# Performance work log

Measured on AMD Instinct MI355X. Metric: run time of the kernel, lower is better.

## Reference

```python
import jax, jax.numpy as jnp
import numpy as np

B, S, D = 2, 2048, 768
H, STRIDE = 12, 8
HD = D // H  # 64


def setup_inputs() -> dict:
    key = jax.random.key(0)
    k0, k1, k2 = jax.random.split(key, 3)
    x = jax.random.normal(k0, (B, S, D), dtype=jnp.float32)
    qkv_w = jax.random.normal(k1, (3 * D, D), dtype=jnp.float32) * 0.02
    qkv_b = jnp.zeros((3 * D,), dtype=jnp.float32)
    out_w = jax.random.normal(k2, (D, D), dtype=jnp.float32) * 0.02
    out_b = jnp.zeros((D,), dtype=jnp.float32)
    return {"x": x, "qkv_w": qkv_w, "qkv_b": qkv_b, "out_w": out_w, "out_b": out_b}


def _stride_mask(S, stride, causal):
    i = jnp.arange(S)[:, None]
    j = jnp.arange(S)[None, :]
    strided = (j % stride == 0)
    if causal:
        strided = strided & (j <= i)
    # diagonal always attended; previous token attended for i > 0
    return strided | (j == i) | (j == i - 1)


def reference(x, qkv_w, qkv_b, out_w, out_b):
    Bx, Sx, Dx = x.shape
    qkv = x @ qkv_w.T + qkv_b                      # [B,S,3D]
    qkv = qkv.reshape(Bx, Sx, 3, H, HD)
    q, k, v = jnp.transpose(qkv, (2, 0, 3, 1, 4))  # each [B,H,S,HD]
    scale = HD ** -0.5
    attn = jnp.einsum('bhid,bhjd->bhij', q, k) * scale  # [B,H,S,S]
    mask = _stride_mask(Sx, STRIDE, True)          # [S,S] bool
    attn = jnp.where(mask[None, None], attn, -jnp.inf)
    a = jax.nn.softmax(attn, axis=-1)
    # every row has at least the diagonal unmasked, so no NaN rows;
    # nan_to_num kept for exact parity with the torch module
    a = jnp.nan_to_num(a, nan=0.0)
    out = jnp.einsum('bhij,bhjd->bhid', a, v)      # [B,H,S,HD]
    out = jnp.transpose(out, (0, 2, 1, 3)).reshape(Bx, Sx, Dx)
    return out @ out_w.T + out_b
```

## Files before the change

### kernel.cpp

```cpp
#include <hip/hip_runtime.h>
#include <hip/hip_bf16.h>
#include <stdint.h>

#define H_   12
#define S_   2048
#define D_   768
#define HD_  64
#define MS_  256

typedef __bf16 bf16_8 __attribute__((ext_vector_type(8)));
typedef float  f32_4  __attribute__((ext_vector_type(4)));

typedef __attribute__((address_space(1))) void* gas_ptr;
typedef __attribute__((address_space(3))) void* las_ptr;

__device__ __forceinline__ void g2l16(const void* g, void* l) {
  __builtin_amdgcn_global_load_lds((gas_ptr)g, (las_ptr)l, 16, 0, 0);
}

__device__ __forceinline__ f32_4 mfma16(bf16_8 a, bf16_8 b, f32_4 c) {
  return __builtin_amdgcn_mfma_f32_16x16x32_bf16(a, b, c, 0, 0, 0);
}

__device__ __forceinline__ bf16_8 ld8(const __hip_bfloat16* p) {
  return *reinterpret_cast<const bf16_8*>(p);
}

__global__ __launch_bounds__(256) void cvt3_f32_bf16(
    const float* __restrict__ a, const float* __restrict__ b,
    const float* __restrict__ c, __hip_bfloat16* __restrict__ out,
    int na4, int nb4) {
  const int t = blockIdx.x * 256 + threadIdx.x;
  float4 f;
  if (t < na4)            f = reinterpret_cast<const float4*>(a)[t];
  else if (t < na4 + nb4) f = reinterpret_cast<const float4*>(b)[t - na4];
  else                    f = reinterpret_cast<const float4*>(c)[t - na4 - nb4];
  union { __hip_bfloat16 h[4]; ushort4 u; } p;
  p.h[0] = __float2bfloat16(f.x);
  p.h[1] = __float2bfloat16(f.y);
  p.h[2] = __float2bfloat16(f.z);
  p.h[3] = __float2bfloat16(f.w);
  reinterpret_cast<ushort4*>(out)[t] = p.u;
}

template <int MODE, int BN>
__global__ __launch_bounds__(256, 2) void gemm_bt(
    const __hip_bfloat16* __restrict__ A, const __hip_bfloat16* __restrict__ B,
    const float* __restrict__ bias,
    __hip_bfloat16* __restrict__ O0, __hip_bfloat16* __restrict__ O1,
    __hip_bfloat16* __restrict__ O2, __hip_bfloat16* __restrict__ O3,
    __hip_bfloat16* __restrict__ O4, float* __restrict__ OF,
    int M, int N, int K) {
  constexpr int NTJ = BN / 32;
  __shared__ __bf16 sA[128 * 32];
  __shared__ __bf16 sB[BN * 32];
  const int tid  = threadIdx.x;
  const int lane = tid & 63;
  const int wv   = tid >> 6;
  const int m0 = blockIdx.y * 128;
  const int n0 = blockIdx.x * BN;
  const int wr = (wv >> 1) * 64;
  const int wc = (wv & 1) * (BN / 2);

  f32_4 acc[4][NTJ] = {};

  const __hip_bfloat16* aS = A + (size_t)(m0 + (tid >> 2)) * K + ((tid & 3) << 3);
  const __hip_bfloat16* bS = B + (size_t)(n0 + (tid >> 2)) * K + ((tid & 3) << 3);
  const size_t half = (size_t)64 * K;
  __bf16* dA  = &sA[tid * 8];
  __bf16* dA2 = &sA[tid * 8 + 2048];
  __bf16* dB  = &sB[tid * 8];
  __bf16* dB2 = &sB[tid * 8 + 2048];

  const int fr = lane & 15;
  const int kq = (lane >> 4) << 3;

  for (int k0 = 0; k0 < K; k0 += 32) {
    g2l16(aS, dA);
    g2l16(aS + half, dA2);
    g2l16(bS, dB);
    if constexpr (BN == 128) g2l16(bS + half, dB2);
    aS += 32;
    bS += 32;
    __syncthreads();
    bf16_8 af[4], bfm[NTJ];
#pragma unroll
    for (int t = 0; t < 4; ++t)
      af[t] = *reinterpret_cast<const bf16_8*>(&sA[(wr + t * 16 + fr) * 32 + kq]);
#pragma unroll
    for (int t = 0; t < NTJ; ++t)
      bfm[t] = *reinterpret_cast<const bf16_8*>(&sB[(wc + t * 16 + fr) * 32 + kq]);
#pragma unroll
    for (int ti = 0; ti < 4; ++ti)
#pragma unroll
      for (int tj = 0; tj < NTJ; ++tj)
        acc[ti][tj] = mfma16(af[ti], bfm[tj], acc[ti][tj]);
    __syncthreads();
  }

  const int crow = (lane >> 4) << 2;
  const int ccol = lane & 15;
#pragma unroll
  for (int ti = 0; ti < 4; ++ti) {
    const int gmb = m0 + wr + ti * 16 + crow;
#pragma unroll
    for (int tj = 0; tj < NTJ; ++tj) {
      const int gn = n0 + wc + tj * 16 + ccol;
      const float bv = bias[gn];
      if (MODE == 0) {
        const int t   = gn / D_;
        const int rem = gn - t * D_;
        const int hh = rem >> 6, dd = rem & 63;
        if (t < 2) {
          __hip_bfloat16* dst = (t == 0) ? O0 : O1;
#pragma unroll
          for (int r = 0; r < 4; ++r) {
            const int gm = gmb + r;
            const int bb = gm >> 11, ss = gm & (S_ - 1);
            const __hip_bfloat16 hv = __float2bfloat16(acc[ti][tj][r] + bv);
            dst[(((size_t)(bb * H_ + hh) << 11) + ss) * HD_ + dd] = hv;
            if (t == 1 && r == 0 && (gmb & 7) == 0)
              O4[(((size_t)(bb * H_ + hh)) * MS_ + (ss >> 3)) * HD_ + dd] = hv;
          }
        } else {
          const int bb = gmb >> 11, ss = gmb & (S_ - 1);
          union { ushort4 u; __hip_bfloat16 h[4]; } pk;
#pragma unroll
          for (int r = 0; r < 4; ++r) pk.h[r] = __float2bfloat16(acc[ti][tj][r] + bv);
          const size_t rowb = ((size_t)(bb * H_ + hh) * HD_ + dd);
          *reinterpret_cast<ushort4*>(O2 + rowb * S_ + ss) = pk.u;
          if ((ss & 7) == 0) O3[rowb * MS_ + (ss >> 3)] = pk.h[0];
        }
      } else {
#pragma unroll
        for (int r = 0; r < 4; ++r)
          OF[(size_t)(gmb + r) * D_ + gn] = acc[ti][tj][r] + bv;
      }
    }
  }
}

__global__ __launch_bounds__(256) void attn_mfma(
    const __hip_bfloat16* __restrict__ Q, const __hip_bfloat16* __restrict__ Kb,
    const __hip_bfloat16* __restrict__ Ks, const __hip_bfloat16* __restrict__ VT,
    const __hip_bfloat16* __restrict__ VsT, __hip_bfloat16* __restrict__ ctx) {
  __shared__ __bf16 pt[4][16 * 40];
  const int lane = threadIdx.x & 63;
  const int wv   = threadIdx.x >> 6;
  const int task = blockIdx.x * 4 + wv;
  const int bh   = task >> 7;
  const int i0   = (task & 127) << 4;
  const int lr   = lane & 15;
  const int quad = lane >> 4;
  const float SC = 0.125f * 1.44269504088896340736f;

  const __hip_bfloat16* Kh  = Kb  + ((size_t)bh << 11) * HD_;
  const __hip_bfloat16* Ksh = Ks  + (size_t)bh * MS_ * HD_;
  const __hip_bfloat16* VTh = VT  + (size_t)bh * HD_ * S_;
  const __hip_bfloat16* Vsh = VsT + (size_t)bh * HD_ * MS_;
  __bf16* ptw = pt[wv];

  const __hip_bfloat16* qp = Q + (((size_t)bh << 11) + i0 + lr) * HD_ + quad * 8;
  const bf16_8 qf0 = ld8(qp);
  const bf16_8 qf1 = ld8(qp + 32);

  const __bf16 one = (__bf16)1.0f;
  const bf16_8 onesf = {one, one, one, one, one, one, one, one};

  f32_4 Lacc = {}, oacc[4];
#pragma unroll
  for (int ct = 0; ct < 4; ++ct) oacc[ct] = f32_4{0.f, 0.f, 0.f, 0.f};

  const int mmax  = (i0 + 15) >> 3;
  const int nstr  = (mmax >> 5) + 1;
  const int jbase = (i0 >= 8) ? (i0 - 8) : 0;

  auto load_chunk = [&](int c, bf16_8 (&kf)[2][2], bf16_8 (&vf)[4]) {
    if (c < nstr) {
      const int mb = c << 5;
#pragma unroll
      for (int t = 0; t < 2; ++t) {
        const __hip_bfloat16* kp = Ksh + (size_t)(mb + t * 16 + lr) * HD_ + quad * 8;
        kf[t][0] = ld8(kp);
        kf[t][1] = ld8(kp + 32);
      }
#pragma unroll
      for (int ct = 0; ct < 4; ++ct)
        vf[ct] = ld8(Vsh + (size_t)(ct * 16 + lr) * MS_ + mb + quad * 8);
    } else {
#pragma unroll
      for (int t = 0; t < 2; ++t) {
        const int j  = jbase + t * 16 + lr;
        const int jr = (j < S_) ? j : (S_ - 1);
        const __hip_bfloat16* kp = Kh + (size_t)jr * HD_ + quad * 8;
        kf[t][0] = ld8(kp);
        kf[t][1] = ld8(kp + 32);
      }
      const int vs0 = jbase + quad * 8;
      const int vs  = (vs0 <= S_ - 8) ? vs0 : (S_ - 8);
#pragma unroll
      for (int ct = 0; ct < 4; ++ct)
        vf[ct] = ld8(VTh + (size_t)(ct * 16 + lr) * S_ + vs);
    }
  };

  bf16_8 kf[2][2], vf[4], kf2[2][2], vf2[4];
  load_chunk(0, kf, vf);

  for (int c = 0; c <= nstr; ++c) {
    if (c < nstr) load_chunk(c + 1, kf2, vf2);

    const bool strided = (c < nstr);
    const int  mb      = c << 5;

    f32_4 s0 = {}, s1 = {};
    s0 = mfma16(qf0, kf[0][0], s0);
    s0 = mfma16(qf1, kf[0][1], s0);
    s1 = mfma16(qf0, kf[1][0], s1);
    s1 = mfma16(qf1, kf[1][1], s1);

#pragma unroll
    for (int r = 0; r < 4; ++r) {
      const int i = i0 + quad * 4 + r;
      bool v0, v1;
      if (strided) {
        v0 = ((mb + lr) << 3) <= i;
        v1 = ((mb + 16 + lr) << 3) <= i;
      } else {
        const int j0 = jbase + lr, j1 = jbase + 16 + lr;
        v0 = (j0 == i || j0 == i - 1) && (j0 & 7);
        v1 = (j1 == i || j1 == i - 1) && (j1 & 7);
      }
      s0[r] = v0 ? exp2f(fminf(s0[r] * SC, 63.f)) : 0.f;
      s1[r] = v1 ? exp2f(fminf(s1[r] * SC, 63.f)) : 0.f;
    }

#pragma unroll
    for (int r = 0; r < 4; ++r) {
      const int row = quad * 4 + r;
      ptw[row * 40 + lr]      = (__bf16)__float2bfloat16(s0[r]);
      ptw[row * 40 + 16 + lr] = (__bf16)__float2bfloat16(s1[r]);
    }
    const bf16_8 pf = *reinterpret_cast<const bf16_8*>(&ptw[lr * 40 + quad * 8]);

#pragma unroll
    for (int ct = 0; ct < 4; ++ct) oacc[ct] = mfma16(pf, vf[ct], oacc[ct]);
    Lacc = mfma16(pf, onesf, Lacc);

    if (c < nstr) {
#pragma unroll
      for (int t = 0; t < 2; ++t) { kf[t][0] = kf2[t][0]; kf[t][1] = kf2[t][1]; }
#pragma unroll
      for (int ct = 0; ct < 4; ++ct) vf[ct] = vf2[ct];
    }
  }

  const int b = bh / H_;
  const int h = bh - b * H_;
  f32_4 inv;
#pragma unroll
  for (int r = 0; r < 4; ++r) inv[r] = 1.f / Lacc[r];
#pragma unroll
  for (int r = 0; r < 4; ++r) {
    const int i = i0 + quad * 4 + r;
    __hip_bfloat16* cp = ctx + ((size_t)(b * S_ + i)) * D_ + h * HD_ + lr;
#pragma unroll
    for (int ct = 0; ct < 4; ++ct)
      cp[ct * 16] = __float2bfloat16(oacc[ct][r] * inv[r]);
  }
}

extern "C" void kernel_launch(void* const* d_in, const int* in_sizes, int n_in,
                              void* d_out, int out_size, void* d_ws, size_t ws_size,
                              hipStream_t stream) {
  const float* x    = (const float*)d_in[0];
  const float* qkvw = (const float*)d_in[1];
  const float* qkvb = (const float*)d_in[2];
  const float* outw = (const float*)d_in[3];
  const float* outb = (const float*)d_in[4];
  float* out = (float*)d_out;

  const size_t NX  = (size_t)2 * S_ * D_;
  const size_t NW1 = (size_t)3 * D_ * D_;
  const size_t NW2 = (size_t)D_ * D_;
  const size_t NVS = (size_t)2 * H_ * HD_ * MS_;

  __hip_bfloat16* xb  = (__hip_bfloat16*)d_ws;
  __hip_bfloat16* w1b = xb + NX;
  __hip_bfloat16* w2b = w1b + NW1;
  __hip_bfloat16* q   = w2b + NW2;
  __hip_bfloat16* k   = q + NX;
  __hip_bfloat16* vt  = k + NX;
  __hip_bfloat16* vst = vt + NX;
  __hip_bfloat16* ks  = vst + NVS;
  __hip_bfloat16* ctx = ks + NVS;

  const int na4 = (int)(NX / 4), nb4 = (int)(NW1 / 4), nc4 = (int)(NW2 / 4);
  cvt3_f32_bf16<<<dim3((na4 + nb4 + nc4) / 256), 256, 0, stream>>>(
      x, qkvw, outw, xb, na4, nb4);

  gemm_bt<0, 128><<<dim3(2304 / 128, 4096 / 128), 256, 0, stream>>>(
      xb, w1b, qkvb, q, k, vt, vst, ks, nullptr, 4096, 2304, 768);

  attn_mfma<<<dim3(2 * H_ * S_ / 16 / 4), 256, 0, stream>>>(q, k, ks, vt, vst, ctx);

  gemm_bt<1, 64><<<dim3(768 / 64, 4096 / 128), 256, 0, stream>>>(
      ctx, w2b, outb, nullptr, nullptr, nullptr, nullptr, nullptr,
      out, 4096, 768, 768);
}
```

Before: 151.9 us.

## Store V row-major and transpose the local band through LDS in attention

The QKV GEMM epilogue now writes V in the same row-major [B,H,S,HD] layout as Q and K instead of a transposed [HD,S] layout with strided 4-element stores. The attention kernel stages the 32-row local V band into a per-wave LDS buffer and gathers the transposed MFMA fragments from there. The local-band chunk is also split out of the strided loop, removing the per-iteration branch on mask type. This trades scattered global stores in the GEMM for an extra 16 KB of LDS per block and element-wise LDS gathers in attention, which may reduce occupancy.

```diff
diff --git a/kernel.cpp b/kernel.cpp
--- a/kernel.cpp
+++ b/kernel.cpp
@@ -111,25 +111,19 @@
         const int t   = gn / D_;
         const int rem = gn - t * D_;
         const int hh = rem >> 6, dd = rem & 63;
-        if (t < 2) {
-          __hip_bfloat16* dst = (t == 0) ? O0 : O1;
-#pragma unroll
-          for (int r = 0; r < 4; ++r) {
-            const int gm = gmb + r;
-            const int bb = gm >> 11, ss = gm & (S_ - 1);
-            const __hip_bfloat16 hv = __float2bfloat16(acc[ti][tj][r] + bv);
-            dst[(((size_t)(bb * H_ + hh) << 11) + ss) * HD_ + dd] = hv;
-            if (t == 1 && r == 0 && (gmb & 7) == 0)
+        __hip_bfloat16* dst = (t == 0) ? O0 : (t == 1) ? O1 : O2;
+#pragma unroll
+        for (int r = 0; r < 4; ++r) {
+          const int gm = gmb + r;
+          const int bb = gm >> 11, ss = gm & (S_ - 1);
+          const __hip_bfloat16 hv = __float2bfloat16(acc[ti][tj][r] + bv);
+          dst[(((size_t)(bb * H_ + hh) << 11) + ss) * HD_ + dd] = hv;
+          if (r == 0 && (gmb & 7) == 0) {
+            if (t == 1)
               O4[(((size_t)(bb * H_ + hh)) * MS_ + (ss >> 3)) * HD_ + dd] = hv;
+            else if (t == 2)
+              O3[((size_t)(bb * H_ + hh) * HD_ + dd) * MS_ + (ss >> 3)] = hv;
           }
-        } else {
-          const int bb = gmb >> 11, ss = gmb & (S_ - 1);
-          union { ushort4 u; __hip_bfloat16 h[4]; } pk;
-#pragma unroll
-          for (int r = 0; r < 4; ++r) pk.h[r] = __float2bfloat16(acc[ti][tj][r] + bv);
-          const size_t rowb = ((size_t)(bb * H_ + hh) * HD_ + dd);
-          *reinterpret_cast<ushort4*>(O2 + rowb * S_ + ss) = pk.u;
-          if ((ss & 7) == 0) O3[rowb * MS_ + (ss >> 3)] = pk.h[0];
         }
       } else {
 #pragma unroll
@@ -142,9 +136,10 @@
 
 __global__ __launch_bounds__(256) void attn_mfma(
     const __hip_bfloat16* __restrict__ Q, const __hip_bfloat16* __restrict__ Kb,
-    const __hip_bfloat16* __restrict__ Ks, const __hip_bfloat16* __restrict__ VT,
+    const __hip_bfloat16* __restrict__ Ks, const __hip_bfloat16* __restrict__ Vr,
     const __hip_bfloat16* __restrict__ VsT, __hip_bfloat16* __restrict__ ctx) {
   __shared__ __bf16 pt[4][16 * 40];
+  __shared__ __bf16 vb[4][32 * 64];
   const int lane = threadIdx.x & 63;
   const int wv   = threadIdx.x >> 6;
   const int task = blockIdx.x * 4 + wv;
@@ -156,9 +151,31 @@
 
   const __hip_bfloat16* Kh  = Kb  + ((size_t)bh << 11) * HD_;
   const __hip_bfloat16* Ksh = Ks  + (size_t)bh * MS_ * HD_;
-  const __hip_bfloat16* VTh = VT  + (size_t)bh * HD_ * S_;
+  const __hip_bfloat16* Vrh = Vr  + ((size_t)bh << 11) * HD_;
   const __hip_bfloat16* Vsh = VsT + (size_t)bh * HD_ * MS_;
   __bf16* ptw = pt[wv];
+  __bf16* vbw = vb[wv];
+
+  const int jbase = (i0 >= 8) ? (i0 - 8) : 0;
+
+#pragma unroll
+  for (int it = 0; it < 4; ++it) {
+    const int cidx = it * 64 + lane;
+    const int row = cidx >> 3, seg = cidx & 7;
+    const int j  = jbase + row;
+    const int jr = (j < S_) ? j : (S_ - 1);
+    *reinterpret_cast<bf16_8*>(vbw + row * 64 + seg * 8) =
+        ld8(Vrh + (size_t)jr * HD_ + seg * 8);
+  }
+  bf16_8 kb_[2][2];
+#pragma unroll
+  for (int t = 0; t < 2; ++t) {
+    const int j  = jbase + t * 16 + lr;
+    const int jr = (j < S_) ? j : (S_ - 1);
+    const __hip_bfloat16* kp = Kh + (size_t)jr * HD_ + quad * 8;
+    kb_[t][0] = ld8(kp);
+    kb_[t][1] = ld8(kp + 32);
+  }
 
   const __hip_bfloat16* qp = Q + (((size_t)bh << 11) + i0 + lr) * HD_ + quad * 8;
   const bf16_8 qf0 = ld8(qp);
@@ -171,47 +188,41 @@
 #pragma unroll
   for (int ct = 0; ct < 4; ++ct) oacc[ct] = f32_4{0.f, 0.f, 0.f, 0.f};
 
-  const int mmax  = (i0 + 15) >> 3;
-  const int nstr  = (mmax >> 5) + 1;
-  const int jbase = (i0 >= 8) ? (i0 - 8) : 0;
-
-  auto load_chunk = [&](int c, bf16_8 (&kf)[2][2], bf16_8 (&vf)[4]) {
-    if (c < nstr) {
-      const int mb = c << 5;
-#pragma unroll
-      for (int t = 0; t < 2; ++t) {
-        const __hip_bfloat16* kp = Ksh + (size_t)(mb + t * 16 + lr) * HD_ + quad * 8;
-        kf[t][0] = ld8(kp);
-        kf[t][1] = ld8(kp + 32);
-      }
-#pragma unroll
-      for (int ct = 0; ct < 4; ++ct)
-        vf[ct] = ld8(Vsh + (size_t)(ct * 16 + lr) * MS_ + mb + quad * 8);
-    } else {
-#pragma unroll
-      for (int t = 0; t < 2; ++t) {
-        const int j  = jbase + t * 16 + lr;
-        const int jr = (j < S_) ? j : (S_ - 1);
-        const __hip_bfloat16* kp = Kh + (size_t)jr * HD_ + quad * 8;
-        kf[t][0] = ld8(kp);
-        kf[t][1] = ld8(kp + 32);
-      }
-      const int vs0 = jbase + quad * 8;
-      const int vs  = (vs0 <= S_ - 8) ? vs0 : (S_ - 8);
-#pragma unroll
-      for (int ct = 0; ct < 4; ++ct)
-        vf[ct] = ld8(VTh + (size_t)(ct * 16 + lr) * S_ + vs);
-    }
+  const int mmax = (i0 + 15) >> 3;
+  const int nstr = (mmax >> 5) + 1;
+
+  auto load_str = [&](int c, bf16_8 (&kf)[2][2], bf16_8 (&vf)[4]) {
+    const int mb = c << 5;
+#pragma unroll
+    for (int t = 0; t < 2; ++t) {
+      const __hip_bfloat16* kp = Ksh + (size_t)(mb + t * 16 + lr) * HD_ + quad * 8;
+      kf[t][0] = ld8(kp);
+      kf[t][1] = ld8(kp + 32);
+    }
+#pragma unroll
+    for (int ct = 0; ct < 4; ++ct)
+      vf[ct] = ld8(Vsh + (size_t)(ct * 16 + lr) * MS_ + mb + quad * 8);
   };
 
+  auto softmax_pv = [&](f32_4& s0, f32_4& s1, const bf16_8 (&vf)[4]) {
+#pragma unroll
+    for (int r = 0; r < 4; ++r) {
+      const int row = quad * 4 + r;
+      ptw[row * 40 + lr]      = (__bf16)__float2bfloat16(s0[r]);
+      ptw[row * 40 + 16 + lr] = (__bf16)__float2bfloat16(s1[r]);
+    }
+    const bf16_8 pf = *reinterpret_cast<const bf16_8*>(&ptw[lr * 40 + quad * 8]);
+#pragma unroll
+    for (int ct = 0; ct < 4; ++ct) oacc[ct] = mfma16(pf, vf[ct], oacc[ct]);
+    Lacc = mfma16(pf, onesf, Lacc);
+  };
+
   bf16_8 kf[2][2], vf[4], kf2[2][2], vf2[4];
-  load_chunk(0, kf, vf);
-
-  for (int c = 0; c <= nstr; ++c) {
-    if (c < nstr) load_chunk(c + 1, kf2, vf2);
-
-    const bool strided = (c < nstr);
-    const int  mb      = c << 5;
+  load_str(0, kf, vf);
+  for (int c = 0; c < nstr; ++c) {
+    const bool more = (c + 1 < nstr);
+    if (more) load_str(c + 1, kf2, vf2);
+    const int mb = c << 5;
 
     f32_4 s0 = {}, s1 = {};
     s0 = mfma16(qf0, kf[0][0], s0);
@@ -222,37 +233,48 @@
 #pragma unroll
     for (int r = 0; r < 4; ++r) {
       const int i = i0 + quad * 4 + r;
-      bool v0, v1;
-      if (strided) {
-        v0 = ((mb + lr) << 3) <= i;
-        v1 = ((mb + 16 + lr) << 3) <= i;
-      } else {
-        const int j0 = jbase + lr, j1 = jbase + 16 + lr;
-        v0 = (j0 == i || j0 == i - 1) && (j0 & 7);
-        v1 = (j1 == i || j1 == i - 1) && (j1 & 7);
-      }
+      const bool v0 = ((mb + lr) << 3) <= i;
+      const bool v1 = ((mb + 16 + lr) << 3) <= i;
       s0[r] = v0 ? exp2f(fminf(s0[r] * SC, 63.f)) : 0.f;
       s1[r] = v1 ? exp2f(fminf(s1[r] * SC, 63.f)) : 0.f;
     }
+    softmax_pv(s0, s1, vf);
+
+    if (more) {
+#pragma unroll
+      for (int t = 0; t < 2; ++t) { kf[t][0] = kf2[t][0]; kf[t][1] = kf2[t][1]; }
+#pragma unroll
+      for (int ct = 0; ct < 4; ++ct) vf[ct] = vf2[ct];
+    }
+  }
+
+  {
+    f32_4 s0 = {}, s1 = {};
+    s0 = mfma16(qf0, kb_[0][0], s0);
+    s0 = mfma16(qf1, kb_[0][1], s0);
+    s1 = mfma16(qf0, kb_[1][0], s1);
+    s1 = mfma16(qf1, kb_[1][1], s1);
 
 #pragma unroll
     for (int r = 0; r < 4; ++r) {
-      const int row = quad * 4 + r;
-      ptw[row * 40 + lr]      = (__bf16)__float2bfloat16(s0[r]);
-      ptw[row * 40 + 16 + lr] = (__bf16)__float2bfloat16(s1[r]);
-    }
-    const bf16_8 pf = *reinterpret_cast<const bf16_8*>(&ptw[lr * 40 + quad * 8]);
-
-#pragma unroll
-    for (int ct = 0; ct < 4; ++ct) oacc[ct] = mfma16(pf, vf[ct], oacc[ct]);
-    Lacc = mfma16(pf, onesf, Lacc);
-
-    if (c < nstr) {
-#pragma unroll
-      for (int t = 0; t < 2; ++t) { kf[t][0] = kf2[t][0]; kf[t][1] = kf2[t][1]; }
-#pragma unroll
-      for (int ct = 0; ct < 4; ++ct) vf[ct] = vf2[ct];
-    }
+      const int i = i0 + quad * 4 + r;
+      const int j0 = jbase + lr, j1 = jbase + 16 + lr;
+      const bool v0 = (j0 == i || j0 == i - 1) && (j0 & 7);
+      const bool v1 = (j1 == i || j1 == i - 1) && (j1 & 7);
+      s0[r] = v0 ? exp2f(fminf(s0[r] * SC, 63.f)) : 0.f;
+      s1[r] = v1 ? exp2f(fminf(s1[r] * SC, 63.f)) : 0.f;
+    }
+
+    bf16_8 vfb[4];
+#pragma unroll
+    for (int ct = 0; ct < 4; ++ct) {
+      bf16_8 tmp;
+#pragma unroll
+      for (int e = 0; e < 8; ++e)
+        tmp[e] = vbw[(quad * 8 + e) * 64 + ct * 16 + lr];
+      vfb[ct] = tmp;
+    }
+    softmax_pv(s0, s1, vfb);
   }
 
   const int b = bh / H_;
@@ -290,8 +312,8 @@
   __hip_bfloat16* w2b = w1b + NW1;
   __hip_bfloat16* q   = w2b + NW2;
   __hip_bfloat16* k   = q + NX;
-  __hip_bfloat16* vt  = k + NX;
-  __hip_bfloat16* vst = vt + NX;
+  __hip_bfloat16* vr  = k + NX;
+  __hip_bfloat16* vst = vr + NX;
   __hip_bfloat16* ks  = vst + NVS;
   __hip_bfloat16* ctx = ks + NVS;
 
@@ -300,9 +322,9 @@
       x, qkvw, outw, xb, na4, nb4);
 
   gemm_bt<0, 128><<<dim3(2304 / 128, 4096 / 128), 256, 0, stream>>>(
-      xb, w1b, qkvb, q, k, vt, vst, ks, nullptr, 4096, 2304, 768);
-
-  attn_mfma<<<dim3(2 * H_ * S_ / 16 / 4), 256, 0, stream>>>(q, k, ks, vt, vst, ctx);
+      xb, w1b, qkvb, q, k, vr, vst, ks, nullptr, 4096, 2304, 768);
+
+  attn_mfma<<<dim3(2 * H_ * S_ / 16 / 4), 256, 0, stream>>>(q, k, ks, vr, vst, ctx);
 
   gemm_bt<1, 64><<<dim3(768 / 64, 4096 / 128), 256, 0, stream>>>(
       ctx, w2b, outb, nullptr, nullptr, nullptr, nullptr, nullptr,
```

Result: no change. 150.1 us (-1.2%).
